# Kernel optimization log

Measured on AMD Instinct MI355X. Metric: run time of the kernel, lower is better.

## Reference

```python
import jax, jax.numpy as jnp
import numpy as np

NUM_EXPERTS = 8
RANK = 16
TOP_K = 2
SCALING = 32.0 / RANK  # alpha / rank = 2.0
IN_F = 2048
OUT_F = 2048


def setup_inputs() -> dict:
    key = jax.random.key(0)
    k1, k2, k3, k4, k5 = jax.random.split(key, 5)
    B, T = 4, 2048
    x = jax.random.normal(k1, (B, T, IN_F), dtype=jnp.float32)
    # kaiming-uniform-ish scales
    bound_w = 1.0 / np.sqrt(IN_F)
    weight = jax.random.uniform(k2, (OUT_F, IN_F), jnp.float32, -bound_w, bound_w)
    lora_A = jax.random.uniform(k3, (NUM_EXPERTS, RANK, IN_F), jnp.float32, -bound_w, bound_w)
    # lora_B is zero-initialized in the module; use small random values so the
    # expert path is numerically non-trivial for kernel correctness testing.
    lora_B = 0.02 * jax.random.normal(k4, (NUM_EXPERTS, OUT_F, RANK), dtype=jnp.float32)
    router_w = jax.random.uniform(k5, (NUM_EXPERTS, IN_F), jnp.float32, -bound_w, bound_w)
    return {"x": x, "weight": weight, "lora_A": lora_A, "lora_B": lora_B, "router_w": router_w}


def reference(x, weight, lora_A, lora_B, router_w):
    B, T, D = x.shape
    N = B * T
    # base dense projection: [B,T,O]
    base = jnp.einsum('btd,od->bto', x, weight)
    # routing
    logits = jnp.einsum('btd,ed->bte', x, router_w)
    probs = jax.nn.softmax(logits, axis=-1)
    topk_vals, topk_idx = jax.lax.top_k(probs, TOP_K)          # [B,T,K]
    topk_vals = topk_vals / topk_vals.sum(axis=-1, keepdims=True)
    # dense per-token expert weights: zero for non-selected experts -> same math
    # as the per-k gather loop (top_k indices are distinct).
    w_dense = jnp.zeros((N, NUM_EXPERTS), dtype=x.dtype).at[
        jnp.arange(N)[:, None], topk_idx.reshape(N, TOP_K)
    ].set(topk_vals.reshape(N, TOP_K))                          # [N,E]
    x_flat = x.reshape(N, D)
    # low-rank expert path: Ax [N,E,r] is tiny (E*r=128), then weighted combine
    Ax = jnp.einsum('nd,erd->ner', x_flat, lora_A)
    expert_out = jnp.einsum('ner,ne,eor->no', Ax, w_dense, lora_B) * SCALING
    return base + expert_out.reshape(B, T, OUT_F)
```

## Files before the change

kernel.cpp:

```cpp
#include <hip/hip_runtime.h>
#include <hip/hip_bf16.h>
#include <stdint.h>

#define IN_F   2048
#define OUT_F  2048
#define NTOK   8192
#define KAUG   2176
#define RANKE  128
#define SCALING 2.0f
#define NT64   34
#define NITER  17

typedef float  f32x4 __attribute__((ext_vector_type(4)));
typedef __bf16 bf16x8 __attribute__((ext_vector_type(8)));

#define GLOAD(g, l) __builtin_amdgcn_global_load_lds(                                   \
    (const __attribute__((address_space(1))) unsigned int*)(g),                          \
    (__attribute__((address_space(3))) unsigned int*)(l), 16, 0, 0)
#define PIN()    asm volatile("" ::: "memory")
#define BAR()    __builtin_amdgcn_s_barrier()
#define WAITL()  asm volatile("s_waitcnt lgkmcnt(0)" ::: "memory")
#define WAITV0() asm volatile("s_waitcnt vmcnt(0)" ::: "memory")
#define WAITV4() asm volatile("s_waitcnt vmcnt(4)" ::: "memory")
#define WAITV10() asm volatile("s_waitcnt vmcnt(10)" ::: "memory")
#define SB0()    __builtin_amdgcn_sched_barrier(0)

__device__ __forceinline__ unsigned short f2b(float f) {
  union { float f; unsigned u; } v; v.f = f;
  return (unsigned short)((v.u + 0x7FFFu + ((v.u >> 16) & 1u)) >> 16);
}

__device__ __forceinline__ uint4 pack8(float4 a, float4 b) {
  uint4 p;
  p.x = f2b(a.x) | ((unsigned)f2b(a.y) << 16);
  p.y = f2b(a.z) | ((unsigned)f2b(a.w) << 16);
  p.z = f2b(b.x) | ((unsigned)f2b(b.y) << 16);
  p.w = f2b(b.z) | ((unsigned)f2b(b.w) << 16);
  return p;
}

__global__ __launch_bounds__(256)
void k_pre(const float* __restrict__ x, const float* __restrict__ rw,
           const float* __restrict__ wt, const float* __restrict__ lb,
           const float* __restrict__ la,
           unsigned short* __restrict__ Ap, float* __restrict__ wsc,
           unsigned short* __restrict__ Bp, unsigned short* __restrict__ Ac) {
  const int bid = blockIdx.x;
  const int t = threadIdx.x;

  if (bid >= 1024) {
    const int r0 = (bid - 1024) * 16;
    #pragma unroll
    for (int j = 0; j < 16; ++j) {
      int ch = j * 256 + t;
      int row = r0 + (ch >> 8), col8 = ch & 255;
      const float4* src = (const float4*)(la + (size_t)row * IN_F + col8 * 8);
      *(uint4*)(Ac + (size_t)row * IN_F + col8 * 8) = pack8(src[0], src[1]);
    }
    return;
  }

  const int w = t >> 6, l = t & 63;
  const int n0 = bid * 8 + w * 2;

  float4 xr[2][4][2];
  #pragma unroll
  for (int ti = 0; ti < 2; ++ti) {
    const float4* xp = (const float4*)(x + (size_t)(n0 + ti) * IN_F);
    uint4* dst = (uint4*)(Ap + (size_t)(n0 + ti) * KAUG);
    #pragma unroll
    for (int j = 0; j < 4; ++j) {
      int c = j * 64 + l;
      float4 a = xp[2 * c], b = xp[2 * c + 1];
      xr[ti][j][0] = a; xr[ti][j][1] = b;
      dst[c] = pack8(a, b);
    }
  }

  #pragma unroll
  for (int r = 0; r < 2; ++r) {
    const int o = bid * 2 + r;
    const float4* src = (const float4*)(wt + (size_t)o * IN_F + t * 8);
    *(uint4*)(Bp + (size_t)o * KAUG + t * 8) = pack8(src[0], src[1]);
    if (t < RANKE) {
      float v = lb[((size_t)(t >> 4) * OUT_F + o) * 16 + (t & 15)];
      Bp[(size_t)o * KAUG + IN_F + t] = f2b(v);
    }
  }

  float acc[2][8];
  #pragma unroll
  for (int ti = 0; ti < 2; ++ti)
    #pragma unroll
    for (int e = 0; e < 8; ++e) acc[ti][e] = 0.f;
  #pragma unroll
  for (int e = 0; e < 8; ++e) {
    const float4* wp = (const float4*)(rw + (size_t)e * IN_F);
    #pragma unroll
    for (int j = 0; j < 4; ++j) {
      int c = j * 64 + l;
      float4 ba = wp[2 * c], bb = wp[2 * c + 1];
      #pragma unroll
      for (int ti = 0; ti < 2; ++ti) {
        acc[ti][e] += xr[ti][j][0].x * ba.x + xr[ti][j][0].y * ba.y +
                      xr[ti][j][0].z * ba.z + xr[ti][j][0].w * ba.w;
        acc[ti][e] += xr[ti][j][1].x * bb.x + xr[ti][j][1].y * bb.y +
                      xr[ti][j][1].z * bb.z + xr[ti][j][1].w * bb.w;
      }
    }
  }
  #pragma unroll
  for (int ti = 0; ti < 2; ++ti)
    #pragma unroll
    for (int e = 0; e < 8; ++e) {
      #pragma unroll
      for (int msk = 1; msk <= 32; msk <<= 1) acc[ti][e] += __shfl_xor(acc[ti][e], msk);
    }
  #pragma unroll
  for (int ti = 0; ti < 2; ++ti) {
    float m = acc[ti][0];
    #pragma unroll
    for (int e = 1; e < 8; ++e) m = fmaxf(m, acc[ti][e]);
    float ex[8], dn = 0.f;
    #pragma unroll
    for (int e = 0; e < 8; ++e) { ex[e] = expf(acc[ti][e] - m); dn += ex[e]; }
    float inv = 1.f / dn;
    float v1 = -1.f; int i1 = 0;
    #pragma unroll
    for (int e = 0; e < 8; ++e) {
      float p = ex[e] * inv;
      if (p > v1) { v1 = p; i1 = e; }
    }
    float v2 = -1.f; int i2 = 0;
    #pragma unroll
    for (int e = 0; e < 8; ++e) {
      float p = ex[e] * inv;
      if (e != i1 && p > v2) { v2 = p; i2 = e; }
    }
    if ((l >> 3) == ti) {
      int e = l & 7;
      float wsum = v1 + v2;
      float wv = (e == i1) ? (v1 / wsum) : ((e == i2) ? (v2 / wsum) : 0.f);
      wsc[(size_t)(n0 + ti) * 8 + e] = wv * SCALING;
    }
  }
}

__global__ __launch_bounds__(256)
void k_lora(const unsigned short* __restrict__ Ap, const unsigned short* __restrict__ Ac,
            const float* __restrict__ wsc, unsigned short* __restrict__ Vout) {
  __shared__ alignas(16) unsigned short LA[3 * 4096];
  __shared__ alignas(16) unsigned short LB[3 * 16384];
  const int t = threadIdx.x, bm = blockIdx.x;
  const int w = t >> 6, l = t & 63;
  const int lr = l & 15, lq = l >> 4;
  const unsigned short* Ablk = Ap + (size_t)bm * 32 * KAUG;

  f32x4 acc[2][2];
  #pragma unroll
  for (int i = 0; i < 2; ++i)
    #pragma unroll
    for (int j = 0; j < 2; ++j) acc[i][j] = f32x4{0.f, 0.f, 0.f, 0.f};

  auto stg = [&](int buf, int s) {
    #pragma unroll
    for (int i = 0; i < 2; ++i) {
      int slot = i * 256 + t, r = slot >> 4, c = slot & 15;
      GLOAD(Ablk + (size_t)r * KAUG + s * 128 + (c ^ (r & 7)) * 8,
            LA + buf * 4096 + i * 2048 + w * 512);
    }
    #pragma unroll
    for (int i = 0; i < 8; ++i) {
      int slot = i * 256 + t, r = slot >> 4, c = slot & 15;
      GLOAD(Ac + (size_t)r * IN_F + s * 128 + (c ^ (r & 7)) * 8,
            LB + buf * 16384 + i * 2048 + w * 512);
    }
  };

  stg(0, 0); stg(1, 1);
  for (int s = 0; s < 16; ++s) {
    if (s == 15) { WAITV0(); } else { WAITV10(); }
    PIN(); BAR();
    if (s + 2 < 16) stg((s + 2) % 3, s + 2);
    const int buf = s % 3;
    bf16x8 xf[2][2][2], bf[2][2][2];
    #pragma unroll
    for (int kh = 0; kh < 2; ++kh)
      #pragma unroll
      for (int mi = 0; mi < 2; ++mi)
        #pragma unroll
        for (int ks = 0; ks < 2; ++ks) {
          int row = mi * 16 + lr;
          int ch = kh * 8 + ks * 4 + lq;
          xf[kh][mi][ks] = *(const bf16x8*)(LA + buf * 4096 + row * 128 + (ch ^ (row & 7)) * 8);
        }
    #pragma unroll
    for (int kh = 0; kh < 2; ++kh)
      #pragma unroll
      for (int ni = 0; ni < 2; ++ni)
        #pragma unroll
        for (int ks = 0; ks < 2; ++ks) {
          int row = w * 32 + ni * 16 + lr;
          int ch = kh * 8 + ks * 4 + lq;
          bf[kh][ni][ks] = *(const bf16x8*)(LB + buf * 16384 + row * 128 + (ch ^ (row & 7)) * 8);
        }
    #pragma unroll
    for (int kh = 0; kh < 2; ++kh)
      #pragma unroll
      for (int mi = 0; mi < 2; ++mi)
        #pragma unroll
        for (int ni = 0; ni < 2; ++ni)
          #pragma unroll
          for (int ks = 0; ks < 2; ++ks)
            acc[mi][ni] = __builtin_amdgcn_mfma_f32_16x16x32_bf16(
                xf[kh][mi][ks], bf[kh][ni][ks], acc[mi][ni], 0, 0, 0);
  }

  #pragma unroll
  for (int mi = 0; mi < 2; ++mi)
    #pragma unroll
    for (int ni = 0; ni < 2; ++ni)
      #pragma unroll
      for (int j = 0; j < 4; ++j) {
        int row = bm * 32 + mi * 16 + lq * 4 + j;
        int col = w * 32 + ni * 16 + lr;
        float sg = wsc[row * 8 + (col >> 4)];
        Vout[(size_t)row * KAUG + col] = f2b(acc[mi][ni][j] * sg);
      }
}

__global__ __launch_bounds__(512, 2)
void k_main(const unsigned short* __restrict__ A, const unsigned short* __restrict__ B,
            float* __restrict__ out) {
  __shared__ alignas(16) unsigned short LDS[65536];

  const int tid = threadIdx.x;
  const int id = blockIdx.x;
  const int xcd = id & 7, loc = id >> 3;
  const int bm = xcd * 4 + (loc >> 3);
  const int bn = loc & 7;
  const int w = tid >> 6, l = tid & 63;
  const int wr = w >> 2, wc = w & 3;
  const int lr = l & 15, lq = l >> 4, lx = l & 7;

  const unsigned short* Ablk = A + (size_t)bm * 256 * KAUG;
  const unsigned short* Bblk = B + (size_t)bn * 256 * KAUG;

  const size_t gofs0 = (size_t)(tid >> 3) * KAUG + (size_t)(((tid & 7) ^ ((tid >> 3) & 7)) * 8);
  const size_t gofs1 = (size_t)((tid + 512) >> 3) * KAUG +
                       (size_t)((((tid + 512) & 7) ^ (((tid + 512) >> 3) & 7)) * 8);
  unsigned short* const ldsW = LDS + w * 512;

  const int arow = wr * 128 + lr, brow = wc * 64 + lr;
  const int sl0 = (lq ^ lx) * 8, sl1 = ((4 + lq) ^ lx) * 8;

  f32x4 acc[8][4];
  #pragma unroll
  for (int i = 0; i < 8; ++i)
    #pragma unroll
    for (int j = 0; j < 4; ++j) acc[i][j] = f32x4{0.f, 0.f, 0.f, 0.f};
  bf16x8 aF[4][2], bF[4][2];

  auto stage = [&](int isB, int half, int kt) {
    if (kt >= NT64) return;
    const unsigned short* g = (isB ? Bblk : Ablk) + (size_t)(half * 128) * KAUG + (size_t)kt * 64;
    unsigned short* ld = ldsW + isB * 32768 + (kt & 1) * 16384 + half * 8192;
    GLOAD(g + gofs0, ld);
    GLOAD(g + gofs1, ld + 4096);
  };

#define QUAD(MQ, NQ)                                                                     \
  do {                                                                                   \
    _Pragma("unroll") for (int mi_ = 0; mi_ < 4; ++mi_)                                  \
    _Pragma("unroll") for (int ni_ = 0; ni_ < 2; ++ni_)                                  \
    _Pragma("unroll") for (int ks_ = 0; ks_ < 2; ++ks_)                                  \
      acc[(MQ)*4 + mi_][(NQ)*2 + ni_] = __builtin_amdgcn_mfma_f32_16x16x32_bf16(         \
          aF[mi_][ks_], bF[(NQ)*2 + ni_][ks_], acc[(MQ)*4 + mi_][(NQ)*2 + ni_],          \
          0, 0, 0);                                                                      \
  } while (0)

  stage(1, 0, 0); stage(1, 1, 0); stage(0, 0, 0); stage(0, 1, 0);
  stage(1, 0, 1); stage(1, 1, 1);
  WAITV4(); PIN(); BAR();

  for (int i = 0; i < NITER; ++i) {
    const int k1 = 2 * i + 1;
    const int a0 = arow * 64,   b0 = 32768 + brow * 64;
    const int a1 = a0 + 16384,  b1 = b0 + 16384;

    #pragma unroll
    for (int mi = 0; mi < 4; ++mi) {
      aF[mi][0] = *(const bf16x8*)(LDS + a0 + mi * 1024 + sl0);
      aF[mi][1] = *(const bf16x8*)(LDS + a0 + mi * 1024 + sl1);
    }
    #pragma unroll
    for (int ni = 0; ni < 2; ++ni) {
      bF[ni][0] = *(const bf16x8*)(LDS + b0 + ni * 1024 + sl0);
      bF[ni][1] = *(const bf16x8*)(LDS + b0 + ni * 1024 + sl1);
    }
    stage(0, 0, k1);
    PIN(); WAITL(); SB0();
    __builtin_amdgcn_s_setprio(1); QUAD(0, 0); __builtin_amdgcn_s_setprio(0);
    PIN(); BAR();
    #pragma unroll
    for (int ni = 2; ni < 4; ++ni) {
      bF[ni][0] = *(const bf16x8*)(LDS + b0 + ni * 1024 + sl0);
      bF[ni][1] = *(const bf16x8*)(LDS + b0 + ni * 1024 + sl1);
    }
    stage(0, 1, k1);
    PIN(); WAITL(); SB0();
    __builtin_amdgcn_s_setprio(1); QUAD(0, 1); __builtin_amdgcn_s_setprio(0);
    PIN(); BAR();
    #pragma unroll
    for (int mi = 0; mi < 4; ++mi) {
      aF[mi][0] = *(const bf16x8*)(LDS + a0 + (mi + 4) * 1024 + sl0);
      aF[mi][1] = *(const bf16x8*)(LDS + a0 + (mi + 4) * 1024 + sl1);
    }
    stage(1, 0, k1 + 1);
    PIN(); WAITL(); SB0();
    __builtin_amdgcn_s_setprio(1); QUAD(1, 1); __builtin_amdgcn_s_setprio(0);
    PIN(); BAR();
    stage(1, 1, k1 + 1);
    PIN();
    __builtin_amdgcn_s_setprio(1); QUAD(1, 0); __builtin_amdgcn_s_setprio(0);
    PIN();
    if (i == NITER - 1) { WAITV0(); } else { WAITV4(); }
    PIN(); BAR();

    #pragma unroll
    for (int mi = 0; mi < 4; ++mi) {
      aF[mi][0] = *(const bf16x8*)(LDS + a1 + mi * 1024 + sl0);
      aF[mi][1] = *(const bf16x8*)(LDS + a1 + mi * 1024 + sl1);
    }
    #pragma unroll
    for (int ni = 0; ni < 2; ++ni) {
      bF[ni][0] = *(const bf16x8*)(LDS + b1 + ni * 1024 + sl0);
      bF[ni][1] = *(const bf16x8*)(LDS + b1 + ni * 1024 + sl1);
    }
    stage(0, 0, k1 + 1);
    PIN(); WAITL(); SB0();
    __builtin_amdgcn_s_setprio(1); QUAD(0, 0); __builtin_amdgcn_s_setprio(0);
    PIN(); BAR();
    #pragma unroll
    for (int ni = 2; ni < 4; ++ni) {
      bF[ni][0] = *(const bf16x8*)(LDS + b1 + ni * 1024 + sl0);
      bF[ni][1] = *(const bf16x8*)(LDS + b1 + ni * 1024 + sl1);
    }
    stage(0, 1, k1 + 1);
    PIN(); WAITL(); SB0();
    __builtin_amdgcn_s_setprio(1); QUAD(0, 1); __builtin_amdgcn_s_setprio(0);
    PIN(); BAR();
    #pragma unroll
    for (int mi = 0; mi < 4; ++mi) {
      aF[mi][0] = *(const bf16x8*)(LDS + a1 + (mi + 4) * 1024 + sl0);
      aF[mi][1] = *(const bf16x8*)(LDS + a1 + (mi + 4) * 1024 + sl1);
    }
    stage(1, 0, k1 + 2);
    PIN(); WAITL(); SB0();
    __builtin_amdgcn_s_setprio(1); QUAD(1, 1); __builtin_amdgcn_s_setprio(0);
    PIN(); BAR();
    stage(1, 1, k1 + 2);
    PIN();
    __builtin_amdgcn_s_setprio(1); QUAD(1, 0); __builtin_amdgcn_s_setprio(0);
    PIN();
    if (i == NITER - 1) { WAITV0(); } else { WAITV4(); }
    PIN(); BAR();
  }
#undef QUAD

  #pragma unroll
  for (int mi = 0; mi < 8; ++mi)
    #pragma unroll
    for (int ni = 0; ni < 4; ++ni)
      #pragma unroll
      for (int j = 0; j < 4; ++j) {
        int row = bm * 256 + wr * 128 + mi * 16 + lq * 4 + j;
        int col = bn * 256 + wc * 64 + ni * 16 + lr;
        out[(size_t)row * OUT_F + col] = acc[mi][ni][j];
      }
}

extern "C" void kernel_launch(void* const* d_in, const int* in_sizes, int n_in,
                              void* d_out, int out_size, void* d_ws, size_t ws_size,
                              hipStream_t stream) {
  const float* x  = (const float*)d_in[0];
  const float* wt = (const float*)d_in[1];
  const float* la = (const float*)d_in[2];
  const float* lb = (const float*)d_in[3];
  const float* rw = (const float*)d_in[4];
  float* out = (float*)d_out;
  char* ws = (char*)d_ws;

  unsigned short* Ap  = (unsigned short*)ws;
  unsigned short* Bp  = (unsigned short*)(ws + 35651584);
  unsigned short* Ac  = (unsigned short*)(ws + 44564480);
  float*          wsc = (float*)(ws + 45088768);

  k_pre<<<1032, 256, 0, stream>>>(x, rw, wt, lb, la, Ap, wsc, Bp, Ac);
  k_lora<<<NTOK / 32, 256, 0, stream>>>(Ap, Ac, wsc, Ap + IN_F);
  k_main<<<256, 512, 0, stream>>>(Ap, Bp, out);
}
```

Before: 116.8 us.

## Retile main GEMM to 256x128 blocks with 3-stage K=32 LDS pipeline

```diff
diff --git a/kernel.cpp b/kernel.cpp
--- a/kernel.cpp
+++ b/kernel.cpp
@@ -8,8 +8,7 @@
 #define KAUG   2176
 #define RANKE  128
 #define SCALING 2.0f
-#define NT64   34
-#define NITER  17
+#define NT32   68
 
 typedef float  f32x4 __attribute__((ext_vector_type(4)));
 typedef __bf16 bf16x8 __attribute__((ext_vector_type(8)));
@@ -21,7 +20,7 @@
 #define BAR()    __builtin_amdgcn_s_barrier()
 #define WAITL()  asm volatile("s_waitcnt lgkmcnt(0)" ::: "memory")
 #define WAITV0() asm volatile("s_waitcnt vmcnt(0)" ::: "memory")
-#define WAITV4() asm volatile("s_waitcnt vmcnt(4)" ::: "memory")
+#define WAITV6() asm volatile("s_waitcnt vmcnt(6)" ::: "memory")
 #define WAITV10() asm volatile("s_waitcnt vmcnt(10)" ::: "memory")
 #define SB0()    __builtin_amdgcn_sched_barrier(0)
 
@@ -229,144 +228,72 @@
       }
 }
 
-__global__ __launch_bounds__(512, 2)
+__global__ __launch_bounds__(256, 2)
 void k_main(const unsigned short* __restrict__ A, const unsigned short* __restrict__ B,
             float* __restrict__ out) {
-  __shared__ alignas(16) unsigned short LDS[65536];
+  __shared__ alignas(16) unsigned short LA[3 * 8192];
+  __shared__ alignas(16) unsigned short LB[3 * 4096];
 
   const int tid = threadIdx.x;
   const int id = blockIdx.x;
   const int xcd = id & 7, loc = id >> 3;
-  const int bm = xcd * 4 + (loc >> 3);
-  const int bn = loc & 7;
+  const int bm = xcd * 4 + (loc >> 4);
+  const int bn = loc & 15;
   const int w = tid >> 6, l = tid & 63;
-  const int wr = w >> 2, wc = w & 3;
-  const int lr = l & 15, lq = l >> 4, lx = l & 7;
+  const int wr = w >> 1, wc = w & 1;
+  const int lr = l & 15, lq = l >> 4;
 
   const unsigned short* Ablk = A + (size_t)bm * 256 * KAUG;
-  const unsigned short* Bblk = B + (size_t)bn * 256 * KAUG;
-
-  const size_t gofs0 = (size_t)(tid >> 3) * KAUG + (size_t)(((tid & 7) ^ ((tid >> 3) & 7)) * 8);
-  const size_t gofs1 = (size_t)((tid + 512) >> 3) * KAUG +
-                       (size_t)((((tid + 512) & 7) ^ (((tid + 512) >> 3) & 7)) * 8);
-  unsigned short* const ldsW = LDS + w * 512;
-
-  const int arow = wr * 128 + lr, brow = wc * 64 + lr;
-  const int sl0 = (lq ^ lx) * 8, sl1 = ((4 + lq) ^ lx) * 8;
+  const unsigned short* Bblk = B + (size_t)bn * 128 * KAUG;
 
   f32x4 acc[8][4];
   #pragma unroll
   for (int i = 0; i < 8; ++i)
     #pragma unroll
     for (int j = 0; j < 4; ++j) acc[i][j] = f32x4{0.f, 0.f, 0.f, 0.f};
-  bf16x8 aF[4][2], bF[4][2];
-
-  auto stage = [&](int isB, int half, int kt) {
-    if (kt >= NT64) return;
-    const unsigned short* g = (isB ? Bblk : Ablk) + (size_t)(half * 128) * KAUG + (size_t)kt * 64;
-    unsigned short* ld = ldsW + isB * 32768 + (kt & 1) * 16384 + half * 8192;
-    GLOAD(g + gofs0, ld);
-    GLOAD(g + gofs1, ld + 4096);
+  bf16x8 aF[8], bF[4];
+
+  auto stg = [&](int buf, int s) {
+    #pragma unroll
+    for (int i = 0; i < 4; ++i) {
+      int slot = i * 256 + tid, r = slot >> 2, c = slot & 3;
+      GLOAD(Ablk + (size_t)r * KAUG + s * 32 + (c ^ ((r >> 1) & 3)) * 8,
+            LA + buf * 8192 + i * 2048 + w * 512);
+    }
+    #pragma unroll
+    for (int i = 0; i < 2; ++i) {
+      int slot = i * 256 + tid, r = slot >> 2, c = slot & 3;
+      GLOAD(Bblk + (size_t)r * KAUG + s * 32 + (c ^ ((r >> 1) & 3)) * 8,
+            LB + buf * 4096 + i * 2048 + w * 512);
+    }
   };
 
-#define QUAD(MQ, NQ)                                                                     \
-  do {                                                                                   \
-    _Pragma("unroll") for (int mi_ = 0; mi_ < 4; ++mi_)                                  \
-    _Pragma("unroll") for (int ni_ = 0; ni_ < 2; ++ni_)                                  \
-    _Pragma("unroll") for (int ks_ = 0; ks_ < 2; ++ks_)                                  \
-      acc[(MQ)*4 + mi_][(NQ)*2 + ni_] = __builtin_amdgcn_mfma_f32_16x16x32_bf16(         \
-          aF[mi_][ks_], bF[(NQ)*2 + ni_][ks_], acc[(MQ)*4 + mi_][(NQ)*2 + ni_],          \
-          0, 0, 0);                                                                      \
-  } while (0)
-
-  stage(1, 0, 0); stage(1, 1, 0); stage(0, 0, 0); stage(0, 1, 0);
-  stage(1, 0, 1); stage(1, 1, 1);
-  WAITV4(); PIN(); BAR();
-
-  for (int i = 0; i < NITER; ++i) {
-    const int k1 = 2 * i + 1;
-    const int a0 = arow * 64,   b0 = 32768 + brow * 64;
-    const int a1 = a0 + 16384,  b1 = b0 + 16384;
-
-    #pragma unroll
-    for (int mi = 0; mi < 4; ++mi) {
-      aF[mi][0] = *(const bf16x8*)(LDS + a0 + mi * 1024 + sl0);
-      aF[mi][1] = *(const bf16x8*)(LDS + a0 + mi * 1024 + sl1);
-    }
-    #pragma unroll
-    for (int ni = 0; ni < 2; ++ni) {
-      bF[ni][0] = *(const bf16x8*)(LDS + b0 + ni * 1024 + sl0);
-      bF[ni][1] = *(const bf16x8*)(LDS + b0 + ni * 1024 + sl1);
-    }
-    stage(0, 0, k1);
+  stg(0, 0); stg(1, 1);
+  const int sw8 = (lq ^ ((lr >> 1) & 3)) * 8;
+  const int abase = (wr * 128 + lr) * 32 + sw8;
+  const int bbase = (wc * 64 + lr) * 32 + sw8;
+
+  for (int s = 0; s < NT32; ++s) {
+    if (s == NT32 - 1) { WAITV0(); } else { WAITV6(); }
+    PIN(); BAR();
+    if (s + 2 < NT32) stg((s + 2) % 3, s + 2);
+    const int buf = s % 3;
+    #pragma unroll
+    for (int mi = 0; mi < 8; ++mi)
+      aF[mi] = *(const bf16x8*)(LA + buf * 8192 + abase + mi * 512);
+    #pragma unroll
+    for (int ni = 0; ni < 4; ++ni)
+      bF[ni] = *(const bf16x8*)(LB + buf * 4096 + bbase + ni * 512);
     PIN(); WAITL(); SB0();
-    __builtin_amdgcn_s_setprio(1); QUAD(0, 0); __builtin_amdgcn_s_setprio(0);
-    PIN(); BAR();
-    #pragma unroll
-    for (int ni = 2; ni < 4; ++ni) {
-      bF[ni][0] = *(const bf16x8*)(LDS + b0 + ni * 1024 + sl0);
-      bF[ni][1] = *(const bf16x8*)(LDS + b0 + ni * 1024 + sl1);
-    }
-    stage(0, 1, k1);
-    PIN(); WAITL(); SB0();
-    __builtin_amdgcn_s_setprio(1); QUAD(0, 1); __builtin_amdgcn_s_setprio(0);
-    PIN(); BAR();
-    #pragma unroll
-    for (int mi = 0; mi < 4; ++mi) {
-      aF[mi][0] = *(const bf16x8*)(LDS + a0 + (mi + 4) * 1024 + sl0);
-      aF[mi][1] = *(const bf16x8*)(LDS + a0 + (mi + 4) * 1024 + sl1);
-    }
-    stage(1, 0, k1 + 1);
-    PIN(); WAITL(); SB0();
-    __builtin_amdgcn_s_setprio(1); QUAD(1, 1); __builtin_amdgcn_s_setprio(0);
-    PIN(); BAR();
-    stage(1, 1, k1 + 1);
+    __builtin_amdgcn_s_setprio(1);
+    #pragma unroll
+    for (int mi = 0; mi < 8; ++mi)
+      #pragma unroll
+      for (int ni = 0; ni < 4; ++ni)
+        acc[mi][ni] = __builtin_amdgcn_mfma_f32_16x16x32_bf16(aF[mi], bF[ni], acc[mi][ni], 0, 0, 0);
+    __builtin_amdgcn_s_setprio(0);
     PIN();
-    __builtin_amdgcn_s_setprio(1); QUAD(1, 0); __builtin_amdgcn_s_setprio(0);
-    PIN();
-    if (i == NITER - 1) { WAITV0(); } else { WAITV4(); }
-    PIN(); BAR();
-
-    #pragma unroll
-    for (int mi = 0; mi < 4; ++mi) {
-      aF[mi][0] = *(const bf16x8*)(LDS + a1 + mi * 1024 + sl0);
-      aF[mi][1] = *(const bf16x8*)(LDS + a1 + mi * 1024 + sl1);
-    }
-    #pragma unroll
-    for (int ni = 0; ni < 2; ++ni) {
-      bF[ni][0] = *(const bf16x8*)(LDS + b1 + ni * 1024 + sl0);
-      bF[ni][1] = *(const bf16x8*)(LDS + b1 + ni * 1024 + sl1);
-    }
-    stage(0, 0, k1 + 1);
-    PIN(); WAITL(); SB0();
-    __builtin_amdgcn_s_setprio(1); QUAD(0, 0); __builtin_amdgcn_s_setprio(0);
-    PIN(); BAR();
-    #pragma unroll
-    for (int ni = 2; ni < 4; ++ni) {
-      bF[ni][0] = *(const bf16x8*)(LDS + b1 + ni * 1024 + sl0);
-      bF[ni][1] = *(const bf16x8*)(LDS + b1 + ni * 1024 + sl1);
-    }
-    stage(0, 1, k1 + 1);
-    PIN(); WAITL(); SB0();
-    __builtin_amdgcn_s_setprio(1); QUAD(0, 1); __builtin_amdgcn_s_setprio(0);
-    PIN(); BAR();
-    #pragma unroll
-    for (int mi = 0; mi < 4; ++mi) {
-      aF[mi][0] = *(const bf16x8*)(LDS + a1 + (mi + 4) * 1024 + sl0);
-      aF[mi][1] = *(const bf16x8*)(LDS + a1 + (mi + 4) * 1024 + sl1);
-    }
-    stage(1, 0, k1 + 2);
-    PIN(); WAITL(); SB0();
-    __builtin_amdgcn_s_setprio(1); QUAD(1, 1); __builtin_amdgcn_s_setprio(0);
-    PIN(); BAR();
-    stage(1, 1, k1 + 2);
-    PIN();
-    __builtin_amdgcn_s_setprio(1); QUAD(1, 0); __builtin_amdgcn_s_setprio(0);
-    PIN();
-    if (i == NITER - 1) { WAITV0(); } else { WAITV4(); }
-    PIN(); BAR();
-  }
-#undef QUAD
+  }
 
   #pragma unroll
   for (int mi = 0; mi < 8; ++mi)
@@ -375,7 +302,7 @@
       #pragma unroll
       for (int j = 0; j < 4; ++j) {
         int row = bm * 256 + wr * 128 + mi * 16 + lq * 4 + j;
-        int col = bn * 256 + wc * 64 + ni * 16 + lr;
+        int col = bn * 128 + wc * 64 + ni * 16 + lr;
         out[(size_t)row * OUT_F + col] = acc[mi][ni][j];
       }
 }
@@ -398,5 +325,5 @@
 
   k_pre<<<1032, 256, 0, stream>>>(x, rw, wt, lb, la, Ap, wsc, Bp, Ac);
   k_lora<<<NTOK / 32, 256, 0, stream>>>(Ap, Ac, wsc, Ap + IN_F);
-  k_main<<<256, 512, 0, stream>>>(Ap, Bp, out);
-}
+  k_main<<<512, 256, 0, stream>>>(Ap, Bp, out);
+}
```

New measurement: 130.6 us. 1.12x slower.
